# Performance work log

Hardware: AMD Instinct MI355X
Metric: run time of the kernel (lower is better)

## Reference

```python
import jax, jax.numpy as jnp
from jax import lax
import numpy as np

I, H = 512, 1024
B, T = 64, 512


def setup_inputs() -> dict:
    key = jax.random.key(0)
    ks = jax.random.split(key, 16)
    p = lambda k, shape: (jax.random.normal(k, shape, dtype=jnp.float32) * 0.01)
    inp = {
        "inputs": jax.random.normal(ks[0], (B, T, I), dtype=jnp.float32),
        "h_prev_forward": jnp.zeros((B, H), dtype=jnp.float32),
        "h_prev_backward": jnp.zeros((B, H), dtype=jnp.float32),
        # forward-direction params
        "W_hr_f": p(ks[1], (H, H)), "W_xr_f": p(ks[2], (I, H)), "b_r_f": jnp.zeros((H,), jnp.float32),
        "W_hz_f": p(ks[3], (H, H)), "W_xz_f": p(ks[4], (I, H)), "b_z_f": jnp.zeros((H,), jnp.float32),
        "W_hh_f": p(ks[5], (H, H)), "W_xh_f": p(ks[6], (I, H)), "b_h_f": jnp.zeros((H,), jnp.float32),
        # backward-direction params
        "W_hr_b": p(ks[7], (H, H)), "W_xr_b": p(ks[8], (I, H)), "b_r_b": jnp.zeros((H,), jnp.float32),
        "W_hz_b": p(ks[9], (H, H)), "W_xz_b": p(ks[10], (I, H)), "b_z_b": jnp.zeros((H,), jnp.float32),
        "W_hh_b": p(ks[11], (H, H)), "W_xh_b": p(ks[12], (I, H)), "b_h_b": jnp.zeros((H,), jnp.float32),
    }
    return inp


def _gru_dir(x, h0, W_hr, W_xr, b_r, W_hz, W_xz, b_z, W_hh, W_xh, b_h, reverse):
    # Precompute input projections as big GEMMs: (B,T,I)@(I,H) -> (B,T,H)
    xr = jnp.einsum("bti,ih->bth", x, W_xr) + b_r
    xz = jnp.einsum("bti,ih->bth", x, W_xz) + b_z
    xh = jnp.einsum("bti,ih->bth", x, W_xh) + b_h
    # time-major for scan
    xs = (xr.transpose(1, 0, 2), xz.transpose(1, 0, 2), xh.transpose(1, 0, 2))

    def step(h, x_t):
        xr_t, xz_t, xh_t = x_t
        R = jax.nn.sigmoid(h @ W_hr + xr_t)
        Z = jax.nn.sigmoid(h @ W_hz + xz_t)
        # NOTE: original torch code computes (R * h) @ W_hh (left-to-right precedence)
        h_til = jnp.tanh((R * h) @ W_hh + xh_t)
        h_new = Z * h_til + (1.0 - Z) * h
        return h_new, h_new

    _, hs = lax.scan(step, h0, xs, reverse=reverse)  # hs: (T,B,H), time order preserved
    return hs.transpose(1, 0, 2)  # (B,T,H)


def reference(inputs, h_prev_forward, h_prev_backward,
              W_hr_f, W_xr_f, b_r_f, W_hz_f, W_xz_f, b_z_f, W_hh_f, W_xh_f, b_h_f,
              W_hr_b, W_xr_b, b_r_b, W_hz_b, W_xz_b, b_z_b, W_hh_b, W_xh_b, b_h_b):
    h_f = _gru_dir(inputs, h_prev_forward, W_hr_f, W_xr_f, b_r_f,
                   W_hz_f, W_xz_f, b_z_f, W_hh_f, W_xh_f, b_h_f, reverse=False)
    h_b = _gru_dir(inputs, h_prev_backward, W_hr_b, W_xr_b, b_r_b,
                   W_hz_b, W_xz_b, b_z_b, W_hh_b, W_xh_b, b_h_b, reverse=True)
    return jnp.concatenate([h_f, h_b], axis=2)  # (B,T,2H)
```

## Files before the change

kernel.cpp:

```cpp
#include <hip/hip_runtime.h>
#include <hip/hip_bf16.h>
#include <math.h>

typedef __bf16 bf16;
typedef __bf16 bf16x8 __attribute__((ext_vector_type(8)));
typedef __bf16 bf16x4 __attribute__((ext_vector_type(4)));
typedef float f32x4 __attribute__((ext_vector_type(4)));

#define T_LEN 512
#define BATCH 64
#define HDIM  1024
#define IDIM  512

struct Ptr12 { const float* p[12]; };
struct Ptr6  { const float* p[6];  };

__global__ __launch_bounds__(256) void transpose_convert(Ptr12 W, bf16* wt_h, bf16* wt_x) {
    int z = blockIdx.z;
    int K = (z < 6) ? HDIM : IDIM;
    const float* src = W.p[z];
    bf16* dst = (z < 6) ? (wt_h + (size_t)z * HDIM * HDIM)
                        : (wt_x + (size_t)(z - 6) * HDIM * IDIM);
    int n0 = blockIdx.x * 32;
    int k0 = blockIdx.y * 32;
    if (k0 >= K) return;
    __shared__ float tile[32][33];
    int tx = threadIdx.x & 31, ty = threadIdx.x >> 5;
#pragma unroll
    for (int i = 0; i < 32; i += 8)
        tile[ty + i][tx] = src[(size_t)(k0 + ty + i) * HDIM + n0 + tx];
    __syncthreads();
#pragma unroll
    for (int i = 0; i < 32; i += 8)
        dst[(size_t)(n0 + ty + i) * K + k0 + tx] = (bf16)tile[tx][ty + i];
}

__global__ __launch_bounds__(256) void convert_x(const float* __restrict__ x, bf16* __restrict__ xbf) {
    size_t i = ((size_t)blockIdx.x * blockDim.x + threadIdx.x) * 4;
    float4 v = *(const float4*)(x + i);
    bf16x4 o = { (bf16)v.x, (bf16)v.y, (bf16)v.z, (bf16)v.w };
    *(bf16x4*)(xbf + i) = o;
}

__global__ __launch_bounds__(256) void init_h(const float* __restrict__ hf, const float* __restrict__ hb,
                                              bf16* __restrict__ h_cur) {
    int i = blockIdx.x * blockDim.x + threadIdx.x;
    h_cur[i] = (bf16)hf[i];
    h_cur[BATCH * HDIM + i] = (bf16)hb[i];
}

__global__ __launch_bounds__(256) void xproj_gemm(const bf16* __restrict__ xbf,
                                                  const bf16* __restrict__ wt_x,
                                                  Ptr6 biases,
                                                  bf16* __restrict__ XP) {
    int g  = blockIdx.z;
    int m0 = blockIdx.x * 64;
    int n0 = blockIdx.y * 64;
    int w  = threadIdx.x >> 6;
    int l  = threadIdx.x & 63;
    int lm = l & 15, lq = l >> 4;

    const bf16* Wg    = wt_x + (size_t)g * HDIM * IDIM;
    const bf16* Abase = xbf + (size_t)(m0 + 16 * w + lm) * IDIM + lq * 8;
    const bf16* Bbase = Wg + (size_t)(n0 + lm) * IDIM + lq * 8;

    f32x4 acc[4] = {};
#pragma unroll 2
    for (int k = 0; k < IDIM; k += 32) {
        bf16x8 a = *(const bf16x8*)(Abase + k);
#pragma unroll
        for (int nt = 0; nt < 4; nt++) {
            bf16x8 b = *(const bf16x8*)(Bbase + (size_t)nt * 16 * IDIM + k);
            acc[nt] = __builtin_amdgcn_mfma_f32_16x16x32_bf16(a, b, acc[nt], 0, 0, 0);
        }
    }

    const float* bias = biases.p[g];
    int mrow = m0 + 16 * w + lq * 4;
#pragma unroll
    for (int nt = 0; nt < 4; nt++) {
        int n = n0 + nt * 16 + lm;
        float bv = bias[n];
#pragma unroll
        for (int r = 0; r < 4; r++) {
            int m = mrow + r;
            int b_ = m >> 9;
            int t  = m & 511;
            XP[(((size_t)g * T_LEN + t) * BATCH + b_) * HDIM + n] = (bf16)(acc[nt][r] + bv);
        }
    }
}

__global__ __launch_bounds__(256) void gru_phase_a(const bf16* __restrict__ wt_h,
                                                   const bf16* __restrict__ XP,
                                                   const bf16* __restrict__ h_cur,
                                                   bf16* __restrict__ Rh,
                                                   bf16* __restrict__ Zbuf,
                                                   int step) {
    int blk = blockIdx.x;
    int dir = blk >> 7;
    int gb  = (blk >> 6) & 1;
    int s   = blk & 63;
    int n0  = s * 16;
    int t   = dir ? (T_LEN - 1 - step) : step;

    int w = threadIdx.x >> 6, l = threadIdx.x & 63;
    int lm = l & 15, lq = l >> 4;
    int mt   = w & 1;
    int gate = w >> 1;
    int mrowA = gb * 32 + mt * 16 + lm;

    const bf16* h_d = h_cur + (size_t)dir * BATCH * HDIM;
    const bf16* Wp  = wt_h + (size_t)(dir * 3 + gate) * HDIM * HDIM + (size_t)(n0 + lm) * HDIM + lq * 8;
    const bf16* A   = h_d + (size_t)mrowA * HDIM + lq * 8;

    f32x4 acc = {};
#pragma unroll 8
    for (int k = 0; k < HDIM; k += 32) {
        bf16x8 a = *(const bf16x8*)(A + k);
        bf16x8 b = *(const bf16x8*)(Wp + k);
        acc = __builtin_amdgcn_mfma_f32_16x16x32_bf16(a, b, acc, 0, 0, 0);
    }

    const bf16* xp = XP + ((size_t)(dir * 3 + gate) * T_LEN + t) * BATCH * HDIM;
    int n = n0 + lm;
    int brow = gb * 32 + mt * 16 + lq * 4;
#pragma unroll
    for (int r = 0; r < 4; r++) {
        int b_ = brow + r;
        float pre = acc[r] + (float)xp[(size_t)b_ * HDIM + n];
        float gv = 1.0f / (1.0f + __expf(-pre));
        if (gate == 0) {
            float hv = (float)h_d[(size_t)b_ * HDIM + n];
            Rh[(size_t)dir * BATCH * HDIM + (size_t)b_ * HDIM + n] = (bf16)(gv * hv);
        } else {
            Zbuf[(size_t)dir * BATCH * HDIM + (size_t)b_ * HDIM + n] = (bf16)gv;
        }
    }
}

__global__ __launch_bounds__(128) void gru_phase_b(const bf16* __restrict__ wt_h,
                                                   const bf16* __restrict__ XP,
                                                   const bf16* __restrict__ Rh,
                                                   const bf16* __restrict__ Zbuf,
                                                   bf16* __restrict__ h_cur,
                                                   float* __restrict__ out,
                                                   int step) {
    int blk = blockIdx.x;
    int dir = blk >> 7;
    int gb  = (blk >> 6) & 1;
    int s   = blk & 63;
    int n0  = s * 16;
    int t   = dir ? (T_LEN - 1 - step) : step;

    int w = threadIdx.x >> 6, l = threadIdx.x & 63;
    int lm = l & 15, lq = l >> 4;
    int mrowA = gb * 32 + w * 16 + lm;

    const bf16* Rh_d = Rh + (size_t)dir * BATCH * HDIM;
    const bf16* Wp   = wt_h + (size_t)(dir * 3 + 2) * HDIM * HDIM + (size_t)(n0 + lm) * HDIM + lq * 8;
    const bf16* A    = Rh_d + (size_t)mrowA * HDIM + lq * 8;

    f32x4 acc = {};
#pragma unroll 8
    for (int k = 0; k < HDIM; k += 32) {
        bf16x8 a = *(const bf16x8*)(A + k);
        bf16x8 b = *(const bf16x8*)(Wp + k);
        acc = __builtin_amdgcn_mfma_f32_16x16x32_bf16(a, b, acc, 0, 0, 0);
    }

    bf16* h_d = h_cur + (size_t)dir * BATCH * HDIM;
    const bf16* Z_d = Zbuf + (size_t)dir * BATCH * HDIM;
    const bf16* xp = XP + ((size_t)(dir * 3 + 2) * T_LEN + t) * BATCH * HDIM;
    int n = n0 + lm;
    int brow = gb * 32 + w * 16 + lq * 4;
#pragma unroll
    for (int r = 0; r < 4; r++) {
        int b_ = brow + r;
        float pre = acc[r] + (float)xp[(size_t)b_ * HDIM + n];
        float e2x = __expf(2.0f * pre);
        float ht  = (e2x - 1.0f) / (e2x + 1.0f);
        float z   = (float)Z_d[(size_t)b_ * HDIM + n];
        float ho  = (float)h_d[(size_t)b_ * HDIM + n];
        float hn  = z * ht + (1.0f - z) * ho;
        h_d[(size_t)b_ * HDIM + n] = (bf16)hn;
        out[((size_t)b_ * T_LEN + t) * (2 * HDIM) + (size_t)dir * HDIM + n] = hn;
    }
}

extern "C" void kernel_launch(void* const* d_in, const int* in_sizes, int n_in,
                              void* d_out, int out_size, void* d_ws, size_t ws_size,
                              hipStream_t stream) {
    const float* x   = (const float*)d_in[0];
    const float* hpf = (const float*)d_in[1];
    const float* hpb = (const float*)d_in[2];

    unsigned char* ws = (unsigned char*)d_ws;
    size_t off = 0;
    bf16* wt_h = (bf16*)(ws + off); off += (size_t)6 * HDIM * HDIM * 2;
    bf16* wt_x = (bf16*)(ws + off); off += (size_t)6 * HDIM * IDIM * 2;
    bf16* xbf  = (bf16*)(ws + off); off += (size_t)BATCH * T_LEN * IDIM * 2;
    bf16* XP   = (bf16*)(ws + off); off += (size_t)6 * T_LEN * BATCH * HDIM * 2;
    bf16* h_cur = (bf16*)(ws + off); off += (size_t)2 * BATCH * HDIM * 2;
    bf16* Rh    = (bf16*)(ws + off); off += (size_t)2 * BATCH * HDIM * 2;
    bf16* Zbuf  = (bf16*)(ws + off); off += (size_t)2 * BATCH * HDIM * 2;

    float* out = (float*)d_out;

    Ptr12 wp;
    wp.p[0] = (const float*)d_in[3];  wp.p[1] = (const float*)d_in[6];  wp.p[2] = (const float*)d_in[9];
    wp.p[3] = (const float*)d_in[12]; wp.p[4] = (const float*)d_in[15]; wp.p[5] = (const float*)d_in[18];
    wp.p[6] = (const float*)d_in[4];  wp.p[7] = (const float*)d_in[7];  wp.p[8] = (const float*)d_in[10];
    wp.p[9] = (const float*)d_in[13]; wp.p[10] = (const float*)d_in[16]; wp.p[11] = (const float*)d_in[19];
    transpose_convert<<<dim3(32, 32, 12), 256, 0, stream>>>(wp, wt_h, wt_x);

    convert_x<<<16384, 256, 0, stream>>>(x, xbf);

    init_h<<<256, 256, 0, stream>>>(hpf, hpb, h_cur);

    Ptr6 bp;
    bp.p[0] = (const float*)d_in[5];  bp.p[1] = (const float*)d_in[8];  bp.p[2] = (const float*)d_in[11];
    bp.p[3] = (const float*)d_in[14]; bp.p[4] = (const float*)d_in[17]; bp.p[5] = (const float*)d_in[20];
    xproj_gemm<<<dim3(512, 16, 6), 256, 0, stream>>>(xbf, wt_x, bp, XP);

    for (int step = 0; step < T_LEN; ++step) {
        gru_phase_a<<<256, 256, 0, stream>>>(wt_h, XP, h_cur, Rh, Zbuf, step);
        gru_phase_b<<<256, 128, 0, stream>>>(wt_h, XP, Rh, Zbuf, h_cur, out, step);
    }
}
```

Before: 12.32 ms.

## Replace per-step kernel launches with persistent cooperative GRU kernel using grid barriers

Replaces the 1024 per-timestep kernel launches with a single cooperative persistent kernel of 256 blocks. Each block keeps its slice of the recurrent weights resident in LDS, and the two phases are separated by atomic-counter barriers, each scoped to the 64 blocks of one direction and batch half. The Z gate stays in shared memory, and the candidate GEMM is split across two K halves whose partial sums are reduced through LDS. This removes launch overhead and repeated weight reloads from global memory, at the cost of spin-wait barriers and a requirement that all 256 blocks be co-resident.

```diff
diff --git a/kernel.cpp b/kernel.cpp
--- a/kernel.cpp
+++ b/kernel.cpp
@@ -43,10 +43,11 @@
 }
 
 __global__ __launch_bounds__(256) void init_h(const float* __restrict__ hf, const float* __restrict__ hb,
-                                              bf16* __restrict__ h_cur) {
+                                              bf16* __restrict__ h_cur, unsigned* __restrict__ bars) {
     int i = blockIdx.x * blockDim.x + threadIdx.x;
     h_cur[i] = (bf16)hf[i];
     h_cur[BATCH * HDIM + i] = (bf16)hb[i];
+    if (blockIdx.x == 0) bars[threadIdx.x] = 0u;
 }
 
 __global__ __launch_bounds__(256) void xproj_gemm(const bf16* __restrict__ xbf,
@@ -91,100 +92,138 @@
     }
 }
 
-__global__ __launch_bounds__(256) void gru_phase_a(const bf16* __restrict__ wt_h,
-                                                   const bf16* __restrict__ XP,
-                                                   const bf16* __restrict__ h_cur,
-                                                   bf16* __restrict__ Rh,
-                                                   bf16* __restrict__ Zbuf,
-                                                   int step) {
-    int blk = blockIdx.x;
-    int dir = blk >> 7;
-    int gb  = (blk >> 6) & 1;
-    int s   = blk & 63;
-    int n0  = s * 16;
-    int t   = dir ? (T_LEN - 1 - step) : step;
-
-    int w = threadIdx.x >> 6, l = threadIdx.x & 63;
-    int lm = l & 15, lq = l >> 4;
-    int mt   = w & 1;
-    int gate = w >> 1;
-    int mrowA = gb * 32 + mt * 16 + lm;
-
-    const bf16* h_d = h_cur + (size_t)dir * BATCH * HDIM;
-    const bf16* Wp  = wt_h + (size_t)(dir * 3 + gate) * HDIM * HDIM + (size_t)(n0 + lm) * HDIM + lq * 8;
-    const bf16* A   = h_d + (size_t)mrowA * HDIM + lq * 8;
-
-    f32x4 acc = {};
-#pragma unroll 8
-    for (int k = 0; k < HDIM; k += 32) {
-        bf16x8 a = *(const bf16x8*)(A + k);
-        bf16x8 b = *(const bf16x8*)(Wp + k);
-        acc = __builtin_amdgcn_mfma_f32_16x16x32_bf16(a, b, acc, 0, 0, 0);
-    }
-
-    const bf16* xp = XP + ((size_t)(dir * 3 + gate) * T_LEN + t) * BATCH * HDIM;
-    int n = n0 + lm;
-    int brow = gb * 32 + mt * 16 + lq * 4;
-#pragma unroll
-    for (int r = 0; r < 4; r++) {
-        int b_ = brow + r;
-        float pre = acc[r] + (float)xp[(size_t)b_ * HDIM + n];
-        float gv = 1.0f / (1.0f + __expf(-pre));
-        if (gate == 0) {
-            float hv = (float)h_d[(size_t)b_ * HDIM + n];
-            Rh[(size_t)dir * BATCH * HDIM + (size_t)b_ * HDIM + n] = (bf16)(gv * hv);
-        } else {
-            Zbuf[(size_t)dir * BATCH * HDIM + (size_t)b_ * HDIM + n] = (bf16)gv;
-        }
-    }
-}
-
-__global__ __launch_bounds__(128) void gru_phase_b(const bf16* __restrict__ wt_h,
-                                                   const bf16* __restrict__ XP,
-                                                   const bf16* __restrict__ Rh,
-                                                   const bf16* __restrict__ Zbuf,
-                                                   bf16* __restrict__ h_cur,
-                                                   float* __restrict__ out,
-                                                   int step) {
-    int blk = blockIdx.x;
-    int dir = blk >> 7;
-    int gb  = (blk >> 6) & 1;
-    int s   = blk & 63;
-    int n0  = s * 16;
-    int t   = dir ? (T_LEN - 1 - step) : step;
-
-    int w = threadIdx.x >> 6, l = threadIdx.x & 63;
-    int lm = l & 15, lq = l >> 4;
-    int mrowA = gb * 32 + w * 16 + lm;
-
-    const bf16* Rh_d = Rh + (size_t)dir * BATCH * HDIM;
-    const bf16* Wp   = wt_h + (size_t)(dir * 3 + 2) * HDIM * HDIM + (size_t)(n0 + lm) * HDIM + lq * 8;
-    const bf16* A    = Rh_d + (size_t)mrowA * HDIM + lq * 8;
-
-    f32x4 acc = {};
-#pragma unroll 8
-    for (int k = 0; k < HDIM; k += 32) {
-        bf16x8 a = *(const bf16x8*)(A + k);
-        bf16x8 b = *(const bf16x8*)(Wp + k);
-        acc = __builtin_amdgcn_mfma_f32_16x16x32_bf16(a, b, acc, 0, 0, 0);
-    }
-
-    bf16* h_d = h_cur + (size_t)dir * BATCH * HDIM;
-    const bf16* Z_d = Zbuf + (size_t)dir * BATCH * HDIM;
-    const bf16* xp = XP + ((size_t)(dir * 3 + 2) * T_LEN + t) * BATCH * HDIM;
-    int n = n0 + lm;
-    int brow = gb * 32 + w * 16 + lq * 4;
-#pragma unroll
-    for (int r = 0; r < 4; r++) {
-        int b_ = brow + r;
-        float pre = acc[r] + (float)xp[(size_t)b_ * HDIM + n];
-        float e2x = __expf(2.0f * pre);
-        float ht  = (e2x - 1.0f) / (e2x + 1.0f);
-        float z   = (float)Z_d[(size_t)b_ * HDIM + n];
-        float ho  = (float)h_d[(size_t)b_ * HDIM + n];
-        float hn  = z * ht + (1.0f - z) * ho;
-        h_d[(size_t)b_ * HDIM + n] = (bf16)hn;
-        out[((size_t)b_ * T_LEN + t) * (2 * HDIM) + (size_t)dir * HDIM + n] = hn;
+__device__ inline void group_barrier(unsigned* ctr, unsigned target) {
+    __syncthreads();
+    if (threadIdx.x == 0) {
+        __hip_atomic_fetch_add(ctr, 1u, __ATOMIC_ACQ_REL, __HIP_MEMORY_SCOPE_AGENT);
+        while (__hip_atomic_load(ctr, __ATOMIC_ACQUIRE, __HIP_MEMORY_SCOPE_AGENT) < target) { }
+    }
+    __syncthreads();
+}
+
+__global__ __launch_bounds__(256, 1) void gru_persistent(
+        const bf16* __restrict__ wt_h, const bf16* __restrict__ XP,
+        bf16* __restrict__ h_cur, bf16* __restrict__ Rh,
+        float* __restrict__ out, unsigned* __restrict__ bars)
+{
+    __shared__ __align__(16) char  Wl[98304];
+    __shared__ __align__(16) float Part[512];
+    __shared__ __align__(16) float Zs[512];
+
+    const int blk = blockIdx.x;
+    const int dir = blk >> 7;
+    const int gb  = (blk >> 6) & 1;
+    const int s   = blk & 63;
+    const int n0  = s * 16;
+    const int tid = threadIdx.x;
+    const int w   = tid >> 6, l = tid & 63;
+    const int lm  = l & 15, lq = l >> 4;
+
+    for (int gate = 0; gate < 3; ++gate) {
+        const bf16* Wg = wt_h + ((size_t)(dir * 3 + gate) * HDIM + n0) * HDIM;
+        char* dst = Wl + gate * 32768;
+        for (int idx = tid; idx < 2048; idx += 256) {
+            int c = idx & 15, kb = idx >> 4;
+            bf16x8 v = *(const bf16x8*)(Wg + (size_t)c * HDIM + kb * 8);
+            *(bf16x8*)(dst + kb * 256 + c * 16) = v;
+        }
+    }
+    __syncthreads();
+
+    bf16* h_d  = h_cur + (size_t)dir * BATCH * HDIM;
+    bf16* Rh_d = Rh    + (size_t)dir * BATCH * HDIM;
+    unsigned* ctr = bars + (dir * 2 + gb) * 64;
+
+    const int gate = w >> 1;
+    const int mt   = w & 1;
+    const int kh   = w >> 1;
+    const int rowA = gb * 32 + mt * 16 + lm;
+    const int brow = gb * 32 + mt * 16 + lq * 4;
+    const int n    = n0 + lm;
+
+    const char* BlA = Wl + gate * 32768 + lq * 256 + lm * 16;
+    const char* BlB = Wl + 2 * 32768 + kh * 16384 + lq * 256 + lm * 16;
+
+    unsigned bt = 0;
+
+#pragma unroll 1
+    for (int step = 0; step < T_LEN; ++step) {
+        const int t = dir ? (T_LEN - 1 - step) : step;
+
+        {
+            const bf16* A   = h_d + (size_t)rowA * HDIM + lq * 8;
+            const bf16* xpA = XP + ((size_t)(dir * 3 + gate) * T_LEN + t) * BATCH * HDIM;
+            float xpv[4], hvv[4] = {};
+#pragma unroll
+            for (int r = 0; r < 4; ++r)
+                xpv[r] = (float)xpA[(size_t)(brow + r) * HDIM + n];
+            if (gate == 0) {
+#pragma unroll
+                for (int r = 0; r < 4; ++r)
+                    hvv[r] = (float)h_d[(size_t)(brow + r) * HDIM + n];
+            }
+            bf16x8 a[32];
+#pragma unroll
+            for (int i = 0; i < 32; ++i)
+                a[i] = *(const bf16x8*)(A + i * 32);
+            f32x4 acc0 = {}, acc1 = {};
+#pragma unroll
+            for (int i = 0; i < 32; i += 2) {
+                bf16x8 b0 = *(const bf16x8*)(BlA + i * 1024);
+                acc0 = __builtin_amdgcn_mfma_f32_16x16x32_bf16(a[i], b0, acc0, 0, 0, 0);
+                bf16x8 b1 = *(const bf16x8*)(BlA + i * 1024 + 1024);
+                acc1 = __builtin_amdgcn_mfma_f32_16x16x32_bf16(a[i + 1], b1, acc1, 0, 0, 0);
+            }
+            f32x4 acc = acc0 + acc1;
+#pragma unroll
+            for (int r = 0; r < 4; ++r) {
+                float pre = acc[r] + xpv[r];
+                float gv = 1.0f / (1.0f + __expf(-pre));
+                if (gate == 0) {
+                    Rh_d[(size_t)(brow + r) * HDIM + n] = (bf16)(gv * hvv[r]);
+                } else {
+                    Zs[mt * 256 + l * 4 + r] = gv;
+                }
+            }
+        }
+        bt += 64; group_barrier(ctr, bt);
+
+        {
+            const bf16* A = Rh_d + (size_t)rowA * HDIM + kh * 512 + lq * 8;
+            bf16x8 a[16];
+#pragma unroll
+            for (int i = 0; i < 16; ++i)
+                a[i] = *(const bf16x8*)(A + i * 32);
+            f32x4 acc0 = {}, acc1 = {};
+#pragma unroll
+            for (int i = 0; i < 16; i += 2) {
+                bf16x8 b0 = *(const bf16x8*)(BlB + i * 1024);
+                acc0 = __builtin_amdgcn_mfma_f32_16x16x32_bf16(a[i], b0, acc0, 0, 0, 0);
+                bf16x8 b1 = *(const bf16x8*)(BlB + i * 1024 + 1024);
+                acc1 = __builtin_amdgcn_mfma_f32_16x16x32_bf16(a[i + 1], b1, acc1, 0, 0, 0);
+            }
+            f32x4 p = acc0 + acc1;
+            if (kh == 1)
+                *(f32x4*)(&Part[mt * 256 + l * 4]) = p;
+            __syncthreads();
+            if (kh == 0) {
+                const bf16* xpH = XP + ((size_t)(dir * 3 + 2) * T_LEN + t) * BATCH * HDIM;
+                f32x4 q = *(const f32x4*)(&Part[mt * 256 + l * 4]);
+#pragma unroll
+                for (int r = 0; r < 4; ++r) {
+                    int b_ = brow + r;
+                    float pre = p[r] + q[r] + (float)xpH[(size_t)b_ * HDIM + n];
+                    float e2x = __expf(2.0f * pre);
+                    float ht  = (e2x - 1.0f) / (e2x + 1.0f);
+                    float z   = Zs[mt * 256 + l * 4 + r];
+                    float ho  = (float)h_d[(size_t)b_ * HDIM + n];
+                    float hn  = z * ht + (1.0f - z) * ho;
+                    h_d[(size_t)b_ * HDIM + n] = (bf16)hn;
+                    out[((size_t)b_ * T_LEN + t) * (2 * HDIM) + (size_t)dir * HDIM + n] = hn;
+                }
+            }
+        }
+        bt += 64; group_barrier(ctr, bt);
     }
 }
 
@@ -203,7 +242,7 @@
     bf16* XP   = (bf16*)(ws + off); off += (size_t)6 * T_LEN * BATCH * HDIM * 2;
     bf16* h_cur = (bf16*)(ws + off); off += (size_t)2 * BATCH * HDIM * 2;
     bf16* Rh    = (bf16*)(ws + off); off += (size_t)2 * BATCH * HDIM * 2;
-    bf16* Zbuf  = (bf16*)(ws + off); off += (size_t)2 * BATCH * HDIM * 2;
+    unsigned* bars = (unsigned*)(ws + off); off += 1024;
 
     float* out = (float*)d_out;
 
@@ -215,16 +254,14 @@
     transpose_convert<<<dim3(32, 32, 12), 256, 0, stream>>>(wp, wt_h, wt_x);
 
     convert_x<<<16384, 256, 0, stream>>>(x, xbf);
-
-    init_h<<<256, 256, 0, stream>>>(hpf, hpb, h_cur);
+    init_h<<<256, 256, 0, stream>>>(hpf, hpb, h_cur, bars);
 
     Ptr6 bp;
     bp.p[0] = (const float*)d_in[5];  bp.p[1] = (const float*)d_in[8];  bp.p[2] = (const float*)d_in[11];
     bp.p[3] = (const float*)d_in[14]; bp.p[4] = (const float*)d_in[17]; bp.p[5] = (const float*)d_in[20];
     xproj_gemm<<<dim3(512, 16, 6), 256, 0, stream>>>(xbf, wt_x, bp, XP);
 
-    for (int step = 0; step < T_LEN; ++step) {
-        gru_phase_a<<<256, 256, 0, stream>>>(wt_h, XP, h_cur, Rh, Zbuf, step);
-        gru_phase_b<<<256, 128, 0, stream>>>(wt_h, XP, Rh, Zbuf, h_cur, out, step);
-    }
-}
+    void* args[] = { (void*)&wt_h, (void*)&XP, (void*)&h_cur, (void*)&Rh,
+                     (void*)&out, (void*)&bars };
+    (void)hipLaunchCooperativeKernel((void*)gru_persistent, dim3(256), dim3(256), args, 0, stream);
+}
```

After: 18.87 ms. +53.2%, slower.
